# Kernel optimization log

Hardware: AMD Instinct MI355X
Metric: run time of the kernel (lower is better)

## Reference

```python
import jax, jax.numpy as jnp
import numpy as np

PROTO_M = 0.99  # cfg.proto_m
EPS = 1e-12     # F.normalize eps

N, D, C, Q = 256, 128, 1000, 262144


def setup_inputs() -> dict:
    key = jax.random.key(0)
    ks = jax.random.split(key, 8)
    return {
        "q_x": jax.random.normal(ks[0], (N, D), jnp.float32),
        "k_x": jax.random.normal(ks[1], (N, D), jnp.float32),
        "output_x": jax.random.normal(ks[2], (N, C), jnp.float32),
        "queue": jax.random.normal(ks[3], (Q, D), jnp.float32),
        "prototypes": jax.random.normal(ks[4], (C, D), jnp.float32),
        "isID": jnp.zeros((Q,), jnp.float32),
        "Y": jax.random.randint(ks[5], (N,), 0, C),
        "queue_Y": jax.random.randint(ks[6], (Q,), 0, C),
        "ptr": 0,
    }


def _ema_prototypes(prototypes, feats, labels, m):
    """Vectorized equivalent of the sequential per-sample EMA loop:
        for feat, label in zip(feats, labels):
            prototypes[label] = prototypes[label]*m + (1-m)*feat
    Closed form (order-exact, handles duplicate labels):
        proto[c] = m^cnt_c * proto[c] + (1-m) * sum_i m^(cnt_c-1-rank_i) * feat_i
    """
    n = feats.shape[0]
    c = prototypes.shape[0]
    same = labels[:, None] == labels[None, :]                    # [N,N]
    rank = jnp.sum(jnp.tril(same, -1), axis=1).astype(feats.dtype)  # prior same-label occurrences
    cnt = jax.ops.segment_sum(jnp.ones((n,), feats.dtype), labels, num_segments=c)  # [C]
    w = (1.0 - m) * m ** (cnt[labels] - 1.0 - rank)              # [N] per-sample weight
    contrib = jax.ops.segment_sum(w[:, None] * feats, labels, num_segments=c)       # [C,D]
    new = prototypes * (m ** cnt)[:, None] + contrib
    norm = jnp.maximum(jnp.linalg.norm(new, axis=1, keepdims=True), EPS)
    return new / norm  # F.normalize(prototypes, p=2, dim=1)


def reference(q_x, k_x, output_x, queue, prototypes, isID, Y, queue_Y, ptr):
    n = q_x.shape[0]
    q_len = queue.shape[0]
    # prototype EMA scatter + renormalize (buffer update, no grad in torch)
    new_protos = _ema_prototypes(prototypes, q_x, Y, PROTO_M)
    # moco_queue features/targets (queue is detached in torch)
    features = jnp.concatenate([q_x, k_x, queue], axis=0)          # [2N+Q, D]
    targets = jnp.concatenate([Y, Y, queue_Y], axis=0)             # [2N+Q]
    # _dequeue_and_enqueue2 with isid = ones(N)
    new_queue = jax.lax.dynamic_update_slice(queue, k_x, (ptr, 0))
    new_queue_Y = jax.lax.dynamic_update_slice(queue_Y, Y, (ptr,))
    new_isID = jax.lax.dynamic_update_slice(isID, jnp.ones((n,), isID.dtype), (ptr,))
    new_ptr = (ptr + n) % q_len
    return (output_x, features, targets, new_protos, new_queue, new_queue_Y, new_isID, new_ptr)
```

## Files before the change

### kernel.cpp

```cpp
#include <hip/hip_runtime.h>
#include <math.h>

constexpr int  Nn = 256;
constexpr int  Dd = 128;
constexpr int  Cc = 1000;
constexpr int  Qq = 262144;
constexpr float PROTO_M = 0.99f;

typedef float vf4 __attribute__((ext_vector_type(4)));
typedef int   vi4 __attribute__((ext_vector_type(4)));

constexpr long SEG_OUTX  = (long)Nn * Cc / 4;
constexpr long SEG_QX    = (long)Nn * Dd / 4;
constexpr long SEG_QUEUE = (long)Qq * Dd / 4;
constexpr long SEG_TGT   = (long)(2 * Nn + Qq) / 4;
constexpr long SEG_QY    = (long)Qq / 4;

constexpr long OFF_OUTX = 0;
constexpr long OFF_FEAT = (long)Nn * Cc;
constexpr long OFF_TGT  = OFF_FEAT + (long)(2 * Nn + Qq) * Dd;
constexpr long OFF_PROT = OFF_TGT + (2 * Nn + Qq);
constexpr long OFF_NQ   = OFF_PROT + (long)Cc * Dd;
constexpr long OFF_NQY  = OFF_NQ + (long)Qq * Dd;
constexpr long OFF_ISID = OFF_NQY + Qq;
constexpr long OFF_PTR  = OFF_ISID + Qq;

constexpr int  PBLOCKS  = Cc / 2;
constexpr int  OBLOCKS  = 512;
constexpr long CH       = 2560;
constexpr int  QBLOCKS  = (int)((SEG_QUEUE + CH - 1) / CH);
constexpr long OTHER_TOTAL = SEG_OUTX + 2 * SEG_QX + SEG_TGT + 2 * SEG_QY + 1;

__global__ __launch_bounds__(256) void mega_kernel(
    const vf4* __restrict__ q_x4, const vf4* __restrict__ k_x4,
    const vf4* __restrict__ output_x4, const vf4* __restrict__ queue4,
    const float* __restrict__ protos, const vf4* __restrict__ isID4,
    const int* __restrict__ Y, const int* __restrict__ queue_Y,
    const int* __restrict__ ptr_p, float* __restrict__ out)
{
    vf4* out4 = (vf4*)out;
    const int bid = blockIdx.x;
    const int t   = threadIdx.x;

    const int ptr_raw = *ptr_p;
    const int ptr = min(max(ptr_raw, 0), Qq - Nn);

    if (bid < PBLOCKS) {
        const float* q_x = (const float*)q_x4;
        const int grp = t >> 7;
        const int c   = bid * 2 + grp;
        const int d   = t & 127;
        float p = protos[(long)c * Dd + d];
        const float m = PROTO_M, om = 1.0f - PROTO_M;
        for (int i = 0; i < Nn; ++i) {
            int y = Y[i];
            if (y == c) p = m * p + om * q_x[(long)i * Dd + d];
        }
        float s = p * p;
        #pragma unroll
        for (int off = 32; off >= 1; off >>= 1) s += __shfl_xor(s, off);
        __shared__ float ws[4];
        if ((t & 63) == 0) ws[t >> 6] = s;
        __syncthreads();
        float norm = fmaxf(sqrtf(ws[2 * grp] + ws[2 * grp + 1]), 1e-12f);
        out[OFF_PROT + (long)c * Dd + d] = p / norm;
        return;
    }

    if (bid < PBLOCKS + OBLOCKS) {
        const vi4* Y4  = (const vi4*)Y;
        const vi4* qY4 = (const vi4*)queue_Y;
        const long stride = (long)OBLOCKS * 256;
        for (long v = (long)(bid - PBLOCKS) * 256 + t; v < OTHER_TOTAL; v += stride) {
            long r = v;
            if (r < SEG_OUTX) {
                vf4 x = __builtin_nontemporal_load(output_x4 + r);
                __builtin_nontemporal_store(x, out4 + OFF_OUTX / 4 + r);
                continue;
            }
            r -= SEG_OUTX;
            if (r < SEG_QX) {
                vf4 x = q_x4[r];
                __builtin_nontemporal_store(x, out4 + OFF_FEAT / 4 + r);
                continue;
            }
            r -= SEG_QX;
            if (r < SEG_QX) {
                vf4 x = k_x4[r];
                __builtin_nontemporal_store(x, out4 + OFF_FEAT / 4 + SEG_QX + r);
                continue;
            }
            r -= SEG_QX;
            if (r < SEG_TGT) {
                vi4 x;
                if (r < Nn / 4)          x = Y4[r];
                else if (r < 2 * Nn / 4) x = Y4[r - Nn / 4];
                else                     x = qY4[r - 2 * Nn / 4];
                vf4 o = { (float)x.x, (float)x.y, (float)x.z, (float)x.w };
                __builtin_nontemporal_store(o, out4 + OFF_TGT / 4 + r);
                continue;
            }
            r -= SEG_TGT;
            if (r < SEG_QY) {
                vi4 x = qY4[r];
                vf4 o = { (float)x.x, (float)x.y, (float)x.z, (float)x.w };
                long e0 = r << 2;
                if (e0 + 3 >= ptr && e0 < (long)ptr + Nn) {
                    #pragma unroll
                    for (int c2 = 0; c2 < 4; ++c2) {
                        long e = e0 + c2;
                        if (e >= ptr && e < (long)ptr + Nn) o[c2] = (float)Y[e - ptr];
                    }
                }
                __builtin_nontemporal_store(o, out4 + OFF_NQY / 4 + r);
                continue;
            }
            r -= SEG_QY;
            if (r < SEG_QY) {
                vf4 o = __builtin_nontemporal_load(isID4 + r);
                long e0 = r << 2;
                if (e0 + 3 >= ptr && e0 < (long)ptr + Nn) {
                    #pragma unroll
                    for (int c2 = 0; c2 < 4; ++c2) {
                        long e = e0 + c2;
                        if (e >= ptr && e < (long)ptr + Nn) o[c2] = 1.0f;
                    }
                }
                __builtin_nontemporal_store(o, out4 + OFF_ISID / 4 + r);
                continue;
            }
            out[OFF_PTR] = (float)((ptr_raw + Nn) % Qq);
        }
        return;
    }

    {
        vf4* __restrict__ feat4 = out4 + OFF_FEAT / 4 + 2 * SEG_QX;
        vf4* __restrict__ nq4   = out4 + OFF_NQ / 4;
        const long s = (long)(bid - PBLOCKS - OBLOCKS) * CH;
        const long e = min(s + CH, SEG_QUEUE);
        for (long i = s + t; i < e; i += 512) {
            const long j = i + 256;
            vf4 a = __builtin_nontemporal_load(queue4 + i);
            vf4 b = __builtin_nontemporal_load(queue4 + j);
            __builtin_nontemporal_store(a, feat4 + i);
            __builtin_nontemporal_store(b, feat4 + j);
            const int rowa = (int)(i >> 5);
            const int rowb = (int)(j >> 5);
            vf4 na = a, nb = b;
            if (rowa >= ptr && rowa < ptr + Nn)
                na = k_x4[((long)(rowa - ptr) << 5) + (i & 31)];
            if (rowb >= ptr && rowb < ptr + Nn)
                nb = k_x4[((long)(rowb - ptr) << 5) + (j & 31)];
            __builtin_nontemporal_store(na, nq4 + i);
            __builtin_nontemporal_store(nb, nq4 + j);
        }
    }
}

extern "C" void kernel_launch(void* const* d_in, const int* in_sizes, int n_in,
                              void* d_out, int out_size, void* d_ws, size_t ws_size,
                              hipStream_t stream)
{
    const float* q_x      = (const float*)d_in[0];
    const float* k_x      = (const float*)d_in[1];
    const float* output_x = (const float*)d_in[2];
    const float* queue    = (const float*)d_in[3];
    const float* protos   = (const float*)d_in[4];
    const float* isID     = (const float*)d_in[5];
    const int*   Y        = (const int*)d_in[6];
    const int*   queue_Y  = (const int*)d_in[7];
    const int*   ptr_p    = (const int*)d_in[8];
    float* out = (float*)d_out;

    hipLaunchKernelGGL(mega_kernel, dim3(PBLOCKS + OBLOCKS + QBLOCKS), dim3(256), 0, stream,
                       (const vf4*)q_x, (const vf4*)k_x,
                       (const vf4*)output_x, (const vf4*)queue,
                       protos, (const vf4*)isID, Y, queue_Y, ptr_p, out);
}
```

Before: 83.45 us.

## Give every block a share of the queue copy on a fixed 2048-block grid

```diff
diff --git a/kernel.cpp b/kernel.cpp
--- a/kernel.cpp
+++ b/kernel.cpp
@@ -25,13 +25,13 @@
 constexpr long OFF_ISID = OFF_NQY + Qq;
 constexpr long OFF_PTR  = OFF_ISID + Qq;
 
+constexpr int  NBLOCKS  = 2048;
+constexpr long CH       = SEG_QUEUE / NBLOCKS;
 constexpr int  PBLOCKS  = Cc / 2;
 constexpr int  OBLOCKS  = 512;
-constexpr long CH       = 2560;
-constexpr int  QBLOCKS  = (int)((SEG_QUEUE + CH - 1) / CH);
 constexpr long OTHER_TOTAL = SEG_OUTX + 2 * SEG_QX + SEG_TGT + 2 * SEG_QY + 1;
 
-__global__ __launch_bounds__(256) void mega_kernel(
+__global__ __launch_bounds__(256, 8) void mega_kernel(
     const vf4* __restrict__ q_x4, const vf4* __restrict__ k_x4,
     const vf4* __restrict__ output_x4, const vf4* __restrict__ queue4,
     const float* __restrict__ protos, const vf4* __restrict__ isID4,
@@ -64,10 +64,8 @@
         __syncthreads();
         float norm = fmaxf(sqrtf(ws[2 * grp] + ws[2 * grp + 1]), 1e-12f);
         out[OFF_PROT + (long)c * Dd + d] = p / norm;
-        return;
     }
-
-    if (bid < PBLOCKS + OBLOCKS) {
+    else if (bid < PBLOCKS + OBLOCKS) {
         const vi4* Y4  = (const vi4*)Y;
         const vi4* qY4 = (const vi4*)queue_Y;
         const long stride = (long)OBLOCKS * 256;
@@ -131,29 +129,36 @@
             }
             out[OFF_PTR] = (float)((ptr_raw + Nn) % Qq);
         }
-        return;
     }
 
     {
         vf4* __restrict__ feat4 = out4 + OFF_FEAT / 4 + 2 * SEG_QX;
         vf4* __restrict__ nq4   = out4 + OFF_NQ / 4;
-        const long s = (long)(bid - PBLOCKS - OBLOCKS) * CH;
-        const long e = min(s + CH, SEG_QUEUE);
-        for (long i = s + t; i < e; i += 512) {
-            const long j = i + 256;
-            vf4 a = __builtin_nontemporal_load(queue4 + i);
-            vf4 b = __builtin_nontemporal_load(queue4 + j);
-            __builtin_nontemporal_store(a, feat4 + i);
-            __builtin_nontemporal_store(b, feat4 + j);
-            const int rowa = (int)(i >> 5);
-            const int rowb = (int)(j >> 5);
-            vf4 na = a, nb = b;
-            if (rowa >= ptr && rowa < ptr + Nn)
-                na = k_x4[((long)(rowa - ptr) << 5) + (i & 31)];
-            if (rowb >= ptr && rowb < ptr + Nn)
-                nb = k_x4[((long)(rowb - ptr) << 5) + (j & 31)];
-            __builtin_nontemporal_store(na, nq4 + i);
-            __builtin_nontemporal_store(nb, nq4 + j);
+        const long s = (long)bid * CH;
+        #pragma unroll
+        for (int it = 0; it < 4; ++it) {
+            const long base = s + (long)it * 1024 + t;
+            vf4 a0 = __builtin_nontemporal_load(queue4 + base);
+            vf4 a1 = __builtin_nontemporal_load(queue4 + base + 256);
+            vf4 a2 = __builtin_nontemporal_load(queue4 + base + 512);
+            vf4 a3 = __builtin_nontemporal_load(queue4 + base + 768);
+            __builtin_nontemporal_store(a0, feat4 + base);
+            __builtin_nontemporal_store(a1, feat4 + base + 256);
+            __builtin_nontemporal_store(a2, feat4 + base + 512);
+            __builtin_nontemporal_store(a3, feat4 + base + 768);
+            vf4 n0 = a0, n1 = a1, n2 = a2, n3 = a3;
+            const int r0 = (int)(base >> 5);
+            const int r1 = (int)((base + 256) >> 5);
+            const int r2 = (int)((base + 512) >> 5);
+            const int r3 = (int)((base + 768) >> 5);
+            if (r0 >= ptr && r0 < ptr + Nn) n0 = k_x4[((long)(r0 - ptr) << 5) + (base & 31)];
+            if (r1 >= ptr && r1 < ptr + Nn) n1 = k_x4[((long)(r1 - ptr) << 5) + ((base + 256) & 31)];
+            if (r2 >= ptr && r2 < ptr + Nn) n2 = k_x4[((long)(r2 - ptr) << 5) + ((base + 512) & 31)];
+            if (r3 >= ptr && r3 < ptr + Nn) n3 = k_x4[((long)(r3 - ptr) << 5) + ((base + 768) & 31)];
+            __builtin_nontemporal_store(n0, nq4 + base);
+            __builtin_nontemporal_store(n1, nq4 + base + 256);
+            __builtin_nontemporal_store(n2, nq4 + base + 512);
+            __builtin_nontemporal_store(n3, nq4 + base + 768);
         }
     }
 }
@@ -173,7 +178,7 @@
     const int*   ptr_p    = (const int*)d_in[8];
     float* out = (float*)d_out;
 
-    hipLaunchKernelGGL(mega_kernel, dim3(PBLOCKS + OBLOCKS + QBLOCKS), dim3(256), 0, stream,
+    hipLaunchKernelGGL(mega_kernel, dim3(NBLOCKS), dim3(256), 0, stream,
                        (const vf4*)q_x, (const vf4*)k_x,
                        (const vf4*)output_x, (const vf4*)queue,
                        protos, (const vf4*)isID, Y, queue_Y, ptr_p, out);
```

Result: no change. 83.50 us (+0.1%).
